# Performance work log

Measured on AMD Instinct MI355X. Metric: run time of the kernel, lower is better.

Reference implementation:

```python
import jax, jax.numpy as jnp
import numpy as np


def setup_inputs() -> dict:
    key = jax.random.key(0)
    ks = jax.random.split(key, 7)
    B, I, H = 8192, 1024, 1024
    x = jax.random.normal(ks[0], (B, I), dtype=jnp.float32)
    h_prev = jax.random.normal(ks[1], (B, H), dtype=jnp.float32)
    C_prev = jax.random.normal(ks[2], (B, H), dtype=jnp.float32)
    W_f = jax.random.normal(ks[3], (I + H, H), dtype=jnp.float32) * 0.01
    W_i = jax.random.normal(ks[4], (I + H, H), dtype=jnp.float32) * 0.01
    W_C = jax.random.normal(ks[5], (I + H, H), dtype=jnp.float32) * 0.01
    W_o = jax.random.normal(ks[6], (I + H, H), dtype=jnp.float32) * 0.01
    b = jnp.zeros((H,), dtype=jnp.float32)
    return {"x": x, "h_prev": h_prev, "C_prev": C_prev,
            "W_f": W_f, "b_f": b, "W_i": W_i, "b_i": b,
            "W_C": W_C, "b_C": b, "W_o": W_o, "b_o": b}


def reference(x, h_prev, C_prev, W_f, b_f, W_i, b_i, W_C, b_C, W_o, b_o):
    combined = jnp.concatenate([x, h_prev], axis=1)  # [B, I+H]
    # Fuse the four gate GEMMs into one [B, I+H] x [I+H, 4H] matmul.
    W = jnp.concatenate([W_f, W_i, W_o, W_C], axis=1)  # [I+H, 4H]
    b = jnp.concatenate([b_f, b_i, b_o, b_C], axis=0)  # [4H]
    gates = combined @ W + b                            # [B, 4H]
    H = C_prev.shape[1]
    f_t = jax.nn.sigmoid(gates[:, 0:H])
    i_t = jax.nn.sigmoid(gates[:, H:2 * H])
    o_t = jax.nn.sigmoid(gates[:, 2 * H:3 * H])
    C_tilda = jnp.tanh(gates[:, 3 * H:4 * H])
    C_t = f_t * C_prev + i_t * C_tilda
    h_t = o_t * jnp.tanh(C_t)
    return (h_t, C_t)
```

## Files before the change

kernel.cpp:

```cpp
#include <hip/hip_runtime.h>
#include <hip/hip_bf16.h>

#define B_SZ 8192
#define IH   2048
#define H_SZ 1024
#define BM   256
#define BK   32
#define NKT  (IH / BK)
#define WBUF 16384

typedef __attribute__((ext_vector_type(8)))  short  short8;
typedef __attribute__((ext_vector_type(16))) float  floatx16;

static __device__ __forceinline__ ushort f2bf(float f) {
  union { float f; unsigned u; } v; v.f = f;
  unsigned u = v.u;
  u += 0x7fffu + ((u >> 16) & 1u);
  return (ushort)(u >> 16);
}
static __device__ __forceinline__ float sigmoidf_(float x) {
  return 1.0f / (1.0f + __expf(-x));
}
static __device__ __forceinline__ float tanhf_(float x) {
  float ax = fabsf(x);
  float e = __expf(-2.0f * ax);
  float t = (1.0f - e) / (1.0f + e);
  return copysignf(t, x);
}
static __device__ __forceinline__ void gload_lds16(const void* gsrc, void* ldst) {
  __builtin_amdgcn_global_load_lds(
      (__attribute__((address_space(1))) const void*)gsrc,
      (__attribute__((address_space(3))) void*)ldst, 16, 0, 0);
}

__global__ __launch_bounds__(256) void convert_w2_kernel(
    const float* __restrict__ Wf, const float* __restrict__ Wi,
    const float* __restrict__ Wo, const float* __restrict__ Wc,
    ushort* __restrict__ Wt2) {
  __shared__ float tile[64][65];
  const int g  = blockIdx.z;
  const float* W = (g == 0) ? Wf : (g == 1) ? Wi : (g == 2) ? Wo : Wc;
  const int n0 = blockIdx.x * 64;
  const int k0 = blockIdx.y * 64;
  const int tid = threadIdx.x;
#pragma unroll
  for (int i = 0; i < 4; ++i) {
    int c = i * 256 + tid;
    int r = c >> 4, c4 = c & 15;
    float4 v = *(const float4*)(W + (size_t)(k0 + r) * H_SZ + n0 + c4 * 4);
    tile[r][c4 * 4 + 0] = v.x;
    tile[r][c4 * 4 + 1] = v.y;
    tile[r][c4 * 4 + 2] = v.z;
    tile[r][c4 * 4 + 3] = v.w;
  }
  __syncthreads();
#pragma unroll
  for (int i = 0; i < 2; ++i) {
    int u  = i * 256 + tid;
    int kc = u >> 6;
    int n  = u & 63;
    ushort o[8] __attribute__((aligned(16)));
#pragma unroll
    for (int e = 0; e < 8; ++e) o[e] = f2bf(tile[kc * 8 + e][n]);
    ushort* dst = Wt2 + (((size_t)(k0 / 8 + kc) * 4 + g) * 1024 + n0 + n) * 8;
    *(uint4*)dst = *(uint4*)&o[0];
  }
}

__global__ __launch_bounds__(256) void convert_a2_kernel(
    const float* __restrict__ x, const float* __restrict__ hp,
    ushort* __restrict__ Abf2) {
  __shared__ float tile[64][65];
  const int k0 = blockIdx.x * 64;
  const int r0 = blockIdx.y * 64;
  const int tid = threadIdx.x;
  const float* base = (k0 < 1024) ? x : hp;
  const int koff = (k0 < 1024) ? k0 : (k0 - 1024);
#pragma unroll
  for (int i = 0; i < 4; ++i) {
    int c = i * 256 + tid;
    int r = c >> 4, c4 = c & 15;
    float4 v = *(const float4*)(base + (size_t)(r0 + r) * 1024 + koff + c4 * 4);
    tile[r][c4 * 4 + 0] = v.x;
    tile[r][c4 * 4 + 1] = v.y;
    tile[r][c4 * 4 + 2] = v.z;
    tile[r][c4 * 4 + 3] = v.w;
  }
  __syncthreads();
#pragma unroll
  for (int i = 0; i < 2; ++i) {
    int u  = i * 256 + tid;
    int kc = u >> 6;
    int r  = u & 63;
    ushort o[8] __attribute__((aligned(16)));
#pragma unroll
    for (int e = 0; e < 8; ++e) o[e] = f2bf(tile[r][kc * 8 + e]);
    ushort* dst = Abf2 + ((size_t)(k0 / 8 + kc) * 8192 + r0 + r) * 8;
    *(uint4*)dst = *(uint4*)&o[0];
  }
}

__global__ __launch_bounds__(512, 2) void lstm_fused_kernel(
    const float* __restrict__ Cp, const ushort* __restrict__ Wt2,
    const ushort* __restrict__ Abf2,
    const float* __restrict__ bf_, const float* __restrict__ bi_,
    const float* __restrict__ bo_, const float* __restrict__ bc_,
    float* __restrict__ out) {
  __shared__ char lds[2 * WBUF];

  const int bid = blockIdx.x;
  const int wg  = (bid & 7) * 64 + (bid >> 3);
  const int b0  = (wg >> 4) * BM;
  const int n0g = (wg & 15) * 64;

  const int tid = threadIdx.x;
  const int ln  = tid & 63;
  const int wv  = tid >> 6;
  const int wm  = wv >> 1, wn = wv & 1;

  floatx16 acc[2][4];
#pragma unroll
  for (int m = 0; m < 2; ++m)
#pragma unroll
    for (int j = 0; j < 4; ++j)
#pragma unroll
      for (int e = 0; e < 16; ++e) acc[m][j][e] = 0.f;

  const char* Abf2B = (const char*)Abf2;
  const unsigned aG = (unsigned)(ln >> 5) * 131072u +
                      (unsigned)(b0 + wm * 64 + (ln & 31)) * 16u;

  const int bRB = (ln >> 5) * 4096 + (wn * 32 + (ln & 31)) * 16;

  const char* WtB = (const char*)Wt2;
  unsigned wS[2];
#pragma unroll
  for (int i = 0; i < 2; ++i) {
    int c    = 2 * i + (tid >> 8);
    int nrt  = tid & 255;
    wS[i] = (unsigned)c * 65536u + (unsigned)(nrt >> 6) * 16384u +
            (unsigned)(n0g + (nrt & 63)) * 16u;
  }
  const int wdst0 = wv * 1024;

#define STAGE_W(db, ktw)                                                      \
  do {                                                                        \
    gload_lds16(WtB + (wS[0] + (unsigned)(ktw)), lds + (db) + wdst0);         \
    gload_lds16(WtB + (wS[1] + (unsigned)(ktw)), lds + (db) + 8192 + wdst0);  \
  } while (0)

  short8 aFA[2][2], aFB[2][2];
  short8 bFA[4][2], bFB[4][2];
#define LOADA(AF, kta)                                                        \
  do {                                                                        \
    _Pragma("unroll")                                                         \
    for (int mt_ = 0; mt_ < 2; ++mt_)                                         \
      _Pragma("unroll")                                                       \
      for (int ks_ = 0; ks_ < 2; ++ks_)                                       \
        AF[mt_][ks_] = *(const short8*)(Abf2B + (aG + (unsigned)(kta) +       \
                         (unsigned)ks_ * 262144u + (unsigned)mt_ * 512u));    \
  } while (0)
#define RDSET_B(BF, db)                                                       \
  do {                                                                        \
    _Pragma("unroll")                                                         \
    for (int g_ = 0; g_ < 4; ++g_)                                            \
      _Pragma("unroll")                                                       \
      for (int ks_ = 0; ks_ < 2; ++ks_)                                       \
        BF[g_][ks_] = *(const short8*)(lds + (db) + bRB + ks_ * 8192 +        \
                                       g_ * 1024);                            \
  } while (0)
#define MFALL(AF, BF)                                                         \
  do {                                                                        \
    __builtin_amdgcn_s_setprio(1);                                            \
    _Pragma("unroll")                                                         \
    for (int ks_ = 0; ks_ < 2; ++ks_)                                         \
      _Pragma("unroll")                                                       \
      for (int mt_ = 0; mt_ < 2; ++mt_)                                       \
        _Pragma("unroll")                                                     \
        for (int g_ = 0; g_ < 4; ++g_)                                        \
          acc[mt_][g_] = __builtin_amdgcn_mfma_f32_32x32x16_bf16(             \
              AF[mt_][ks_], BF[g_][ks_], acc[mt_][g_], 0, 0, 0);              \
    __builtin_amdgcn_s_setprio(0);                                            \
  } while (0)
#define BAR    __builtin_amdgcn_s_barrier()
#define LGKM0  asm volatile("s_waitcnt lgkmcnt(0)" ::: "memory")
#define VMC0   asm volatile("s_waitcnt vmcnt(0)" ::: "memory")

  STAGE_W(0, 0);
  STAGE_W(WBUF, 262144);
  LOADA(aFA, 0);
  VMC0; BAR;
  RDSET_B(bFA, 0);
  LGKM0; BAR;

#pragma unroll 1
  for (int it = 0; it < NKT / 2; ++it) {
    {
      const unsigned ktaN = (unsigned)((2 * it + 1) & 63) * 524288u;
      const unsigned ktwN = (unsigned)((2 * it + 2) & 63) * 262144u;
      RDSET_B(bFB, WBUF);
      LOADA(aFB, ktaN);
      STAGE_W(0, ktwN);
      MFALL(aFA, bFA);
      LGKM0; VMC0; BAR;
    }
    {
      const unsigned ktaN = (unsigned)((2 * it + 2) & 63) * 524288u;
      const unsigned ktwN = (unsigned)((2 * it + 3) & 63) * 262144u;
      RDSET_B(bFA, 0);
      LOADA(aFA, ktaN);
      STAGE_W(WBUF, ktwN);
      MFALL(aFB, bFB);
      LGKM0; VMC0; BAR;
    }
  }

  const int n = n0g + wn * 32 + (ln & 31);
  const float vbf = bf_[n], vbi = bi_[n], vbo = bo_[n], vbc = bc_[n];
  const int h2 = (ln >> 5) * 4;
  float* outh = out;
  float* outC = out + (size_t)B_SZ * H_SZ;
#pragma unroll
  for (int mt = 0; mt < 2; ++mt) {
#pragma unroll
    for (int reg = 0; reg < 16; ++reg) {
      int row = b0 + wm * 64 + mt * 32 + (reg & 3) + 8 * (reg >> 2) + h2;
      float fg = sigmoidf_(acc[mt][0][reg] + vbf);
      float ig = sigmoidf_(acc[mt][1][reg] + vbi);
      float og = sigmoidf_(acc[mt][2][reg] + vbo);
      float cg = tanhf_  (acc[mt][3][reg] + vbc);
      float cp = Cp[(size_t)row * H_SZ + n];
      float Ct = fg * cp + ig * cg;
      float ht = og * tanhf_(Ct);
      outh[(size_t)row * H_SZ + n] = ht;
      outC[(size_t)row * H_SZ + n] = Ct;
    }
  }
#undef STAGE_W
#undef LOADA
#undef RDSET_B
#undef MFALL
#undef BAR
#undef LGKM0
#undef VMC0
}

extern "C" void kernel_launch(void* const* d_in, const int* in_sizes, int n_in,
                              void* d_out, int out_size, void* d_ws, size_t ws_size,
                              hipStream_t stream) {
  const float* x  = (const float*)d_in[0];
  const float* hp = (const float*)d_in[1];
  const float* Cp = (const float*)d_in[2];
  const float* Wf = (const float*)d_in[3];
  const float* bf = (const float*)d_in[4];
  const float* Wi = (const float*)d_in[5];
  const float* bi = (const float*)d_in[6];
  const float* Wc = (const float*)d_in[7];
  const float* bc = (const float*)d_in[8];
  const float* Wo = (const float*)d_in[9];
  const float* bo = (const float*)d_in[10];

  ushort* Wt2  = (ushort*)d_ws;
  ushort* Abf2 = (ushort*)((char*)d_ws + (16u << 20));

  dim3 gridW(16, 32, 4);
  convert_w2_kernel<<<gridW, 256, 0, stream>>>(Wf, Wi, Wo, Wc, Wt2);
  dim3 gridA(32, 128);
  convert_a2_kernel<<<gridA, 256, 0, stream>>>(x, hp, Abf2);

  lstm_fused_kernel<<<512, 512, 0, stream>>>(Cp, Wt2, Abf2,
                                             bf, bi, bo, bc, (float*)d_out);
}
```

Measured before the change: 170.5 us.

## Load weight fragments directly from global memory, dropping LDS staging and barriers

The fused LSTM GEMM kernel stops staging weight tiles into LDS with global_load_lds. Each wave now loads its B fragments straight from the pre-packed bf16 weight buffer into registers, as it already did for A. This removes LDS usage, all block barriers, the explicit waitcnts and the setprio hints. In exchange, the two waves that share a weight tile each fetch it from global memory, adding L2 traffic, and latency hiding now relies on the compiler's scheduling and register double-buffering.

```diff
diff --git a/kernel.cpp b/kernel.cpp
--- a/kernel.cpp
+++ b/kernel.cpp
@@ -7,7 +7,6 @@
 #define BM   256
 #define BK   32
 #define NKT  (IH / BK)
-#define WBUF 16384
 
 typedef __attribute__((ext_vector_type(8)))  short  short8;
 typedef __attribute__((ext_vector_type(16))) float  floatx16;
@@ -26,11 +25,6 @@
   float e = __expf(-2.0f * ax);
   float t = (1.0f - e) / (1.0f + e);
   return copysignf(t, x);
-}
-static __device__ __forceinline__ void gload_lds16(const void* gsrc, void* ldst) {
-  __builtin_amdgcn_global_load_lds(
-      (__attribute__((address_space(1))) const void*)gsrc,
-      (__attribute__((address_space(3))) void*)ldst, 16, 0, 0);
 }
 
 __global__ __launch_bounds__(256) void convert_w2_kernel(
@@ -106,8 +100,6 @@
     const float* __restrict__ bf_, const float* __restrict__ bi_,
     const float* __restrict__ bo_, const float* __restrict__ bc_,
     float* __restrict__ out) {
-  __shared__ char lds[2 * WBUF];
-
   const int bid = blockIdx.x;
   const int wg  = (bid & 7) * 64 + (bid >> 3);
   const int b0  = (wg >> 4) * BM;
@@ -126,28 +118,12 @@
 #pragma unroll
       for (int e = 0; e < 16; ++e) acc[m][j][e] = 0.f;
 
-  const char* Abf2B = (const char*)Abf2;
+  const char* Ab = (const char*)Abf2;
+  const char* Wb = (const char*)Wt2;
   const unsigned aG = (unsigned)(ln >> 5) * 131072u +
                       (unsigned)(b0 + wm * 64 + (ln & 31)) * 16u;
-
-  const int bRB = (ln >> 5) * 4096 + (wn * 32 + (ln & 31)) * 16;
-
-  const char* WtB = (const char*)Wt2;
-  unsigned wS[2];
-#pragma unroll
-  for (int i = 0; i < 2; ++i) {
-    int c    = 2 * i + (tid >> 8);
-    int nrt  = tid & 255;
-    wS[i] = (unsigned)c * 65536u + (unsigned)(nrt >> 6) * 16384u +
-            (unsigned)(n0g + (nrt & 63)) * 16u;
-  }
-  const int wdst0 = wv * 1024;
-
-#define STAGE_W(db, ktw)                                                      \
-  do {                                                                        \
-    gload_lds16(WtB + (wS[0] + (unsigned)(ktw)), lds + (db) + wdst0);         \
-    gload_lds16(WtB + (wS[1] + (unsigned)(ktw)), lds + (db) + 8192 + wdst0);  \
-  } while (0)
+  const unsigned wG = (unsigned)(ln >> 5) * 65536u +
+                      (unsigned)(n0g + wn * 32 + (ln & 31)) * 16u;
 
   short8 aFA[2][2], aFB[2][2];
   short8 bFA[4][2], bFB[4][2];
@@ -157,21 +133,20 @@
     for (int mt_ = 0; mt_ < 2; ++mt_)                                         \
       _Pragma("unroll")                                                       \
       for (int ks_ = 0; ks_ < 2; ++ks_)                                       \
-        AF[mt_][ks_] = *(const short8*)(Abf2B + (aG + (unsigned)(kta) +       \
+        AF[mt_][ks_] = *(const short8*)(Ab + (aG + (unsigned)(kta) +          \
                          (unsigned)ks_ * 262144u + (unsigned)mt_ * 512u));    \
   } while (0)
-#define RDSET_B(BF, db)                                                       \
+#define LOADB(BF, ktw)                                                        \
   do {                                                                        \
     _Pragma("unroll")                                                         \
     for (int g_ = 0; g_ < 4; ++g_)                                            \
       _Pragma("unroll")                                                       \
       for (int ks_ = 0; ks_ < 2; ++ks_)                                       \
-        BF[g_][ks_] = *(const short8*)(lds + (db) + bRB + ks_ * 8192 +        \
-                                       g_ * 1024);                            \
+        BF[g_][ks_] = *(const short8*)(Wb + (wG + (unsigned)(ktw) +           \
+                         (unsigned)ks_ * 131072u + (unsigned)g_ * 16384u));   \
   } while (0)
 #define MFALL(AF, BF)                                                         \
   do {                                                                        \
-    __builtin_amdgcn_s_setprio(1);                                            \
     _Pragma("unroll")                                                         \
     for (int ks_ = 0; ks_ < 2; ++ks_)                                         \
       _Pragma("unroll")                                                       \
@@ -180,38 +155,26 @@
         for (int g_ = 0; g_ < 4; ++g_)                                        \
           acc[mt_][g_] = __builtin_amdgcn_mfma_f32_32x32x16_bf16(             \
               AF[mt_][ks_], BF[g_][ks_], acc[mt_][g_], 0, 0, 0);              \
-    __builtin_amdgcn_s_setprio(0);                                            \
   } while (0)
-#define BAR    __builtin_amdgcn_s_barrier()
-#define LGKM0  asm volatile("s_waitcnt lgkmcnt(0)" ::: "memory")
-#define VMC0   asm volatile("s_waitcnt vmcnt(0)" ::: "memory")
-
-  STAGE_W(0, 0);
-  STAGE_W(WBUF, 262144);
+
   LOADA(aFA, 0);
-  VMC0; BAR;
-  RDSET_B(bFA, 0);
-  LGKM0; BAR;
+  LOADB(bFA, 0);
 
 #pragma unroll 1
   for (int it = 0; it < NKT / 2; ++it) {
     {
-      const unsigned ktaN = (unsigned)((2 * it + 1) & 63) * 524288u;
-      const unsigned ktwN = (unsigned)((2 * it + 2) & 63) * 262144u;
-      RDSET_B(bFB, WBUF);
-      LOADA(aFB, ktaN);
-      STAGE_W(0, ktwN);
+      const unsigned ka = (unsigned)((2 * it + 1) & 63) * 524288u;
+      const unsigned kw = (unsigned)((2 * it + 1) & 63) * 262144u;
+      LOADA(aFB, ka);
+      LOADB(bFB, kw);
       MFALL(aFA, bFA);
-      LGKM0; VMC0; BAR;
     }
     {
-      const unsigned ktaN = (unsigned)((2 * it + 2) & 63) * 524288u;
-      const unsigned ktwN = (unsigned)((2 * it + 3) & 63) * 262144u;
-      RDSET_B(bFA, 0);
-      LOADA(aFA, ktaN);
-      STAGE_W(WBUF, ktwN);
+      const unsigned ka = (unsigned)((2 * it + 2) & 63) * 524288u;
+      const unsigned kw = (unsigned)((2 * it + 2) & 63) * 262144u;
+      LOADA(aFA, ka);
+      LOADB(bFA, kw);
       MFALL(aFB, bFB);
-      LGKM0; VMC0; BAR;
     }
   }
 
@@ -236,13 +199,9 @@
       outC[(size_t)row * H_SZ + n] = Ct;
     }
   }
-#undef STAGE_W
 #undef LOADA
-#undef RDSET_B
+#undef LOADB
 #undef MFALL
-#undef BAR
-#undef LGKM0
-#undef VMC0
 }
 
 extern "C" void kernel_launch(void* const* d_in, const int* in_sizes, int n_in,
```

Measured after the change: 215.1 us. +26.2%, slower.
